# Performance work log

Measured on AMD Instinct MI355X. Metric: run time of the kernel, lower is better.

The kernel has to match this reference:

```python
import jax, jax.numpy as jnp
import numpy as np

B, T, N, F, O = 4, 8192, 64, 16, 32  # batch, timesteps, vertices, in_feat, out_feat


def setup_inputs() -> dict:
    key = jax.random.key(0)
    ks = jax.random.split(key, 8)
    return {
        "x": jax.random.normal(ks[0], (B, T, N * F), dtype=jnp.float32),
        "adj": jax.random.uniform(ks[1], (N, N), dtype=jnp.float32),
        "W1": jax.random.normal(ks[2], (T,), dtype=jnp.float32) / np.sqrt(T).astype(np.float32),
        "W2": jax.random.normal(ks[3], (F, T), dtype=jnp.float32) / np.sqrt(F).astype(np.float32),
        "W3": jax.random.normal(ks[4], (F,), dtype=jnp.float32) / np.sqrt(F).astype(np.float32),
        "bs": jax.random.normal(ks[5], (1, N, N), dtype=jnp.float32) * 0.02,
        "Vs": jax.random.normal(ks[6], (N, N), dtype=jnp.float32) * 0.02,
        "conv_w": jax.random.normal(ks[7], (O, N * F, 3), dtype=jnp.float32) * 0.02,
    }


def reference(x, adj, W1, W2, W3, bs, Vs, conv_w):
    bz, t, _ = x.shape
    x4 = x.reshape(bz, t, N, F)
    xp = jnp.transpose(x4, (0, 2, 3, 1))  # (B, N, F, T)

    # Spatial attention: S in (B, N, N)
    lhs = jnp.einsum('bnft,t->bnf', xp, W1) @ W2          # (B, N, T)
    rhs = jnp.einsum('f,bnft->bnt', W3, xp)               # (B, N, T)
    product = jnp.einsum('bnt,bmt->bnm', lhs, rhs)        # (B, N, N)
    S = jnp.einsum('nm,bmk->bnk', Vs, jax.nn.sigmoid(product + bs))
    S = jax.nn.softmax(S, axis=1)

    # Apply attention over the vertex dim
    xr = jnp.transpose(x4, (0, 1, 3, 2)).reshape(bz, t * F, N)  # (B, T*F, N)
    xm = jnp.einsum('bpn,bnm->bpm', xr, S)                      # (B, T*F, N)
    xf = jnp.transpose(xm.reshape(bz, t, F, N), (0, 2, 1, 3))   # (B, F, T, N)

    # einsum 'bftn,nn->bftn' == scale by diagonal of adj
    xf = xf * jnp.diagonal(adj)                                 # broadcast over N

    xo = jnp.transpose(xf, (0, 2, 3, 1)).reshape(bz, t, N * F)  # (B, T, N*F)

    # Conv1d(kernel=3, padding=1, no bias), channels-last
    out = jax.lax.conv_general_dilated(
        xo, conv_w,
        window_strides=(1,), padding=((1, 1),),
        dimension_numbers=('NWC', 'OIW', 'NWC'))
    return out  # (B, T, O)
```

## Files before the change

kernel.cpp:

```cpp
#include <hip/hip_runtime.h>
#include <hip/hip_bf16.h>

#define B_ 4
#define T_ 8192
#define N_ 64
#define F_ 16
#define O_ 32

typedef _Float16 half8_t __attribute__((ext_vector_type(8)));
typedef _Float16 half4_t __attribute__((ext_vector_type(4)));
typedef float float4_t __attribute__((ext_vector_type(4)));

#define WS_A1G  0
#define WS_SSC  32768
#define WS_WFT  98304
#define WS_P    884736
#define WS_XH   18874368

#define TB_ 32

__global__ __launch_bounds__(256) void kA2(const float* __restrict__ x,
                                           const float* __restrict__ W1,
                                           const float* __restrict__ W2,
                                           const float* __restrict__ W3,
                                           float* __restrict__ P,
                                           _Float16* __restrict__ xh) {
    __shared__ float w2s[16][TB_ + 1];
    __shared__ float w1s[TB_];
    const int b    = blockIdx.x >> 8;
    const int tile = blockIdx.x & 255;
    const int t0   = tile * TB_;
    const int tid  = threadIdx.x;
    const int fq   = tid & 3;

    for (int i = tid; i < 16 * TB_; i += 256) {
        const int f = i >> 5, r = i & 31;
        w2s[f][r] = W2[f * T_ + t0 + r];
    }
    if (tid < TB_) w1s[tid] = W1[t0 + tid];
    __syncthreads();

    float w3v[4];
#pragma unroll
    for (int j = 0; j < 4; ++j) w3v[j] = W3[fq * 4 + j];

    const float* xbase = x + ((size_t)b * T_ + t0) * 1024 + tid * 4;
    _Float16* xhb = xh + ((size_t)b * (T_ + 2) + t0 + 1) * 1024 + tid * 4;
    float4_t accA = {0.f, 0.f, 0.f, 0.f};
    float4_t accG = {0.f, 0.f, 0.f, 0.f};

#pragma unroll
    for (int rb = 0; rb < TB_; rb += 8) {
        float4_t xv[8];
#pragma unroll
        for (int i = 0; i < 8; ++i)
            xv[i] = *(const float4_t*)(xbase + (size_t)(rb + i) * 1024);

        float v[8];
#pragma unroll
        for (int i = 0; i < 8; ++i)
            v[i] = xv[i][0] * w3v[0] + xv[i][1] * w3v[1]
                 + xv[i][2] * w3v[2] + xv[i][3] * w3v[3];
#pragma unroll
        for (int i = 0; i < 8; ++i) v[i] += __shfl_xor(v[i], 1);
#pragma unroll
        for (int i = 0; i < 8; ++i) v[i] += __shfl_xor(v[i], 2);
#pragma unroll
        for (int i = 0; i < 8; ++i) {
            const float w1r = w1s[rb + i];
#pragma unroll
            for (int j = 0; j < 4; ++j) {
                accA[j] += w1r * xv[i][j];
                accG[j] += w2s[fq * 4 + j][rb + i] * v[i];
            }
        }

#pragma unroll
        for (int i = 0; i < 8; ++i) {
            half4_t hv;
            hv[0] = (_Float16)xv[i][0]; hv[1] = (_Float16)xv[i][1];
            hv[2] = (_Float16)xv[i][2]; hv[3] = (_Float16)xv[i][3];
            *(half4_t*)(xhb + (size_t)(rb + i) * 1024) = hv;
        }
    }

    {
        half4_t z = {(_Float16)0.f, (_Float16)0.f, (_Float16)0.f, (_Float16)0.f};
        if (tile == 0)
            *(half4_t*)(xh + (size_t)b * (T_ + 2) * 1024 + tid * 4) = z;
        if (tile == 255)
            *(half4_t*)(xh + ((size_t)b * (T_ + 2) + T_ + 1) * 1024 + tid * 4) = z;
    }

    float* pb = P + (size_t)blockIdx.x * 2048 + tid * 4;
    *(float4_t*)pb          = accA;
    *(float4_t*)(pb + 1024) = accG;
}

__global__ __launch_bounds__(256) void kR(const float* __restrict__ P,
                                          float* __restrict__ A1G) {
    const int b   = blockIdx.x >> 6;
    const int seg = blockIdx.x & 63;
    const int tid = threadIdx.x;
    const int o4  = tid & 7;
    const int g   = tid >> 3;

    const float* base = P + (size_t)b * 256 * 2048 + seg * 32 + o4 * 4;
    float4_t s = {0.f, 0.f, 0.f, 0.f};
#pragma unroll
    for (int tt = 0; tt < 8; ++tt) {
        float4_t v = *(const float4_t*)(base + (size_t)(g * 8 + tt) * 2048);
        s += v;
    }

    __shared__ float4_t red[32][8];
    red[g][o4] = s;
    __syncthreads();
    if (tid < 8) {
        float4_t t = {0.f, 0.f, 0.f, 0.f};
#pragma unroll
        for (int gg = 0; gg < 32; ++gg) t += red[gg][tid];
        *(float4_t*)(A1G + (size_t)b * 2048 + seg * 32 + tid * 4) = t;
    }
}

__global__ __launch_bounds__(256) void kC(const float* __restrict__ A1G,
                                          const float* __restrict__ bs,
                                          const float* __restrict__ Vs,
                                          const float* __restrict__ adj,
                                          float* __restrict__ Ssc) {
    const int b = blockIdx.x;
    __shared__ float a1[64][17], g[64][17];
    __shared__ float sig[64][64];
    __shared__ float vs[64][64];
    __shared__ float redmx[4][64];
    __shared__ float redsm[4][64];
    const int tid = threadIdx.x;

    for (int i = tid; i < 1024; i += 256) {
        a1[i >> 4][i & 15] = A1G[b * 2048 + i];
        g [i >> 4][i & 15] = A1G[b * 2048 + 1024 + i];
    }
    for (int i = tid; i < 4096; i += 256) vs[i >> 6][i & 63] = Vs[i];
    __syncthreads();

#pragma unroll
    for (int i = 0; i < 16; ++i) {
        const int e = tid + 256 * i, r = e >> 6, c = e & 63;
        float p = 0.f;
#pragma unroll
        for (int f = 0; f < 16; ++f) p += a1[r][f] * g[c][f];
        p += bs[e];
        sig[r][c] = 1.f / (1.f + __expf(-p));
    }
    __syncthreads();

    const int gw = tid >> 6;
    const int c  = tid & 63;
    const int r0 = gw * 16;

    float sc_[64];
#pragma unroll
    for (int m = 0; m < 64; ++m) sc_[m] = sig[m][c];

    float acc[16];
#pragma unroll
    for (int rl = 0; rl < 16; ++rl) {
        const float4_t* vr = (const float4_t*)&vs[r0 + rl][0];
        float sA = 0.f, sB = 0.f, sC = 0.f, sD = 0.f;
#pragma unroll
        for (int m4 = 0; m4 < 4; ++m4) {
            float4_t v0 = vr[m4];
            float4_t v1 = vr[m4 + 4];
            float4_t v2 = vr[m4 + 8];
            float4_t v3 = vr[m4 + 12];
#pragma unroll
            for (int j = 0; j < 4; ++j) {
                sA += v0[j] * sc_[m4 * 4 + j];
                sB += v1[j] * sc_[16 + m4 * 4 + j];
                sC += v2[j] * sc_[32 + m4 * 4 + j];
                sD += v3[j] * sc_[48 + m4 * 4 + j];
            }
        }
        acc[rl] = (sA + sB) + (sC + sD);
    }

    float pmax = -1e30f;
#pragma unroll
    for (int rl = 0; rl < 16; ++rl) pmax = fmaxf(pmax, acc[rl]);
    redmx[gw][c] = pmax;
    __syncthreads();
    const float mx = fmaxf(fmaxf(redmx[0][c], redmx[1][c]),
                           fmaxf(redmx[2][c], redmx[3][c]));

    float psum = 0.f;
#pragma unroll
    for (int rl = 0; rl < 16; ++rl) {
        acc[rl] = __expf(acc[rl] - mx);
        psum += acc[rl];
    }
    redsm[gw][c] = psum;
    __syncthreads();
    const float sum = (redsm[0][c] + redsm[1][c]) + (redsm[2][c] + redsm[3][c]);
    const float scl = adj[c * 64 + c] / sum;

#pragma unroll
    for (int rl = 0; rl < 16; ++rl)
        Ssc[b * 4096 + (r0 + rl) * 64 + c] = acc[rl] * scl;
}

__global__ __launch_bounds__(256) void kD(const float* __restrict__ Ssc,
                                          const float* __restrict__ conv_w,
                                          _Float16* __restrict__ Wft) {
    const int b = blockIdx.x >> 5, o = blockIdx.x & 31;
    __shared__ float ssc[4096];
    __shared__ float cw[3072];
    const int tid = threadIdx.x;
    for (int i = tid; i < 4096; i += 256) ssc[i] = Ssc[b * 4096 + i];
    for (int i = tid; i < 3072; i += 256) cw[i] = conv_w[o * 3072 + i];
    __syncthreads();

    const size_t obase = (size_t)(b * 2 + (o >> 4)) * 49152 + (size_t)(o & 15) * 8;

#pragma unroll
    for (int i = 0; i < 12; ++i) {
        const int e = tid + 256 * i;
        const int k = e >> 10, rem = e & 1023, m = rem >> 4, f = rem & 15;
        float s = 0.f;
#pragma unroll
        for (int n = 0; n < 64; ++n) s += cw[(n * 16 + f) * 3 + k] * ssc[m * 64 + n];
        const size_t wi = obase + (size_t)(e >> 5) * 512
                        + (size_t)(((e >> 3) & 3) * 16) * 8 + (e & 7);
        Wft[wi] = (_Float16)s;
    }
}

__global__ __launch_bounds__(256) void kE16(const _Float16* __restrict__ xh,
                                            const _Float16* __restrict__ Wft,
                                            float* __restrict__ out) {
    const int b    = blockIdx.x >> 7;
    const int tile = blockIdx.x & 127;
    const int wave = threadIdx.x >> 6;
    const int lane = threadIdx.x & 63;
    const int q = lane >> 4, l = lane & 15;
    const int t0 = tile * 64 + wave * 16;

    const _Float16* wb0 = Wft + (size_t)(b * 2)     * 49152 + lane * 8;
    const _Float16* wb1 = Wft + (size_t)(b * 2 + 1) * 49152 + lane * 8;
    const _Float16* xb = xh + ((size_t)b * (T_ + 2) + (t0 + l)) * 1024 + q * 8;

    float4_t acc0 = {0.f, 0.f, 0.f, 0.f};
    float4_t acc1 = {0.f, 0.f, 0.f, 0.f};

#pragma unroll 2
    for (int c = 0; c < 32; ++c) {
        const int c0 = c * 32;
#pragma unroll
        for (int kc = 0; kc < 3; ++kc) {
            const int kk = kc * 32 + c;

            half8_t af  = *(const half8_t*)(xb + (size_t)kc * 1024 + c0);
            half8_t bf0 = *(const half8_t*)(wb0 + (size_t)kk * 512);
            half8_t bf1 = *(const half8_t*)(wb1 + (size_t)kk * 512);

            acc0 = __builtin_amdgcn_mfma_f32_16x16x32_f16(af, bf0, acc0, 0, 0, 0);
            acc1 = __builtin_amdgcn_mfma_f32_16x16x32_f16(af, bf1, acc1, 0, 0, 0);
        }
    }

#pragma unroll
    for (int rg = 0; rg < 4; ++rg) {
        const int t = t0 + q * 4 + rg;
        float* op = out + ((size_t)b * T_ + t) * 32;
        op[l]      = acc0[rg];
        op[16 + l] = acc1[rg];
    }
}

extern "C" void kernel_launch(void* const* d_in, const int* in_sizes, int n_in,
                              void* d_out, int out_size, void* d_ws, size_t ws_size,
                              hipStream_t stream) {
    const float* x      = (const float*)d_in[0];
    const float* adj    = (const float*)d_in[1];
    const float* W1     = (const float*)d_in[2];
    const float* W2     = (const float*)d_in[3];
    const float* W3     = (const float*)d_in[4];
    const float* bs     = (const float*)d_in[5];
    const float* Vs     = (const float*)d_in[6];
    const float* conv_w = (const float*)d_in[7];
    float* out = (float*)d_out;

    char* ws = (char*)d_ws;
    float*    A1G = (float*)(ws + WS_A1G);
    float*    Ssc = (float*)(ws + WS_SSC);
    _Float16* Wft = (_Float16*)(ws + WS_WFT);
    float*    P   = (float*)(ws + WS_P);
    _Float16* xh  = (_Float16*)(ws + WS_XH);

    kA2 <<<B_ * (T_ / TB_), 256, 0, stream>>>(x, W1, W2, W3, P, xh);
    kR  <<<B_ * 64,         256, 0, stream>>>(P, A1G);
    kC  <<<B_,              256, 0, stream>>>(A1G, bs, Vs, adj, Ssc);
    kD  <<<B_ * O_,         256, 0, stream>>>(Ssc, conv_w, Wft);
    kE16<<<B_ * (T_ / 64),  256, 0, stream>>>(xh, Wft, out);
}
```

Before: 283.4 us.

## Fuse attention and weight-folding kernels; split conv GEMM waves by output half

Merges the softmax-attention kernel into the conv-weight folding kernel, with each block recomputing the per-batch attention in shared memory. This removes a launch and the global round trip of the scaled attention matrix. The final MFMA kernel now gives each wave one 16-output half over 16 timesteps, doubling the grid for more parallelism. The cost is redundant attention compute across 32 blocks per batch and duplicated input fragment loads across waves.

New measurement: 299.6 us. 1.06x slower.

```diff
diff --git a/kernel.cpp b/kernel.cpp
--- a/kernel.cpp
+++ b/kernel.cpp
@@ -12,7 +12,6 @@
 typedef float float4_t __attribute__((ext_vector_type(4)));
 
 #define WS_A1G  0
-#define WS_SSC  32768
 #define WS_WFT  98304
 #define WS_P    884736
 #define WS_XH   18874368
@@ -124,24 +123,27 @@
     }
 }
 
-__global__ __launch_bounds__(256) void kC(const float* __restrict__ A1G,
-                                          const float* __restrict__ bs,
-                                          const float* __restrict__ Vs,
-                                          const float* __restrict__ adj,
-                                          float* __restrict__ Ssc) {
-    const int b = blockIdx.x;
-    __shared__ float a1[64][17], g[64][17];
-    __shared__ float sig[64][64];
-    __shared__ float vs[64][64];
-    __shared__ float redmx[4][64];
-    __shared__ float redsm[4][64];
+__global__ __launch_bounds__(256) void kCD(const float* __restrict__ A1G,
+                                           const float* __restrict__ bs,
+                                           const float* __restrict__ Vs,
+                                           const float* __restrict__ adj,
+                                           const float* __restrict__ conv_w,
+                                           _Float16* __restrict__ Wft) {
+    const int b = blockIdx.x >> 5, o = blockIdx.x & 31;
+    __shared__ float smem[10880];
+    float* a1  = smem;
+    float* g   = smem + 1088;
+    float* vs  = smem + 2176;
+    float* sig = smem + 6272;
+    float* rmx = smem + 10368;
+    float* rsm = smem + 10624;
     const int tid = threadIdx.x;
 
     for (int i = tid; i < 1024; i += 256) {
-        a1[i >> 4][i & 15] = A1G[b * 2048 + i];
-        g [i >> 4][i & 15] = A1G[b * 2048 + 1024 + i];
-    }
-    for (int i = tid; i < 4096; i += 256) vs[i >> 6][i & 63] = Vs[i];
+        a1[(i >> 4) * 17 + (i & 15)] = A1G[b * 2048 + i];
+        g [(i >> 4) * 17 + (i & 15)] = A1G[b * 2048 + 1024 + i];
+    }
+    for (int i = tid; i < 4096; i += 256) vs[i] = Vs[i];
     __syncthreads();
 
 #pragma unroll
@@ -149,9 +151,9 @@
         const int e = tid + 256 * i, r = e >> 6, c = e & 63;
         float p = 0.f;
 #pragma unroll
-        for (int f = 0; f < 16; ++f) p += a1[r][f] * g[c][f];
+        for (int f = 0; f < 16; ++f) p += a1[r * 17 + f] * g[c * 17 + f];
         p += bs[e];
-        sig[r][c] = 1.f / (1.f + __expf(-p));
+        sig[r * 64 + c] = 1.f / (1.f + __expf(-p));
     }
     __syncthreads();
 
@@ -161,12 +163,12 @@
 
     float sc_[64];
 #pragma unroll
-    for (int m = 0; m < 64; ++m) sc_[m] = sig[m][c];
+    for (int m = 0; m < 64; ++m) sc_[m] = sig[m * 64 + c];
 
     float acc[16];
 #pragma unroll
     for (int rl = 0; rl < 16; ++rl) {
-        const float4_t* vr = (const float4_t*)&vs[r0 + rl][0];
+        const float4_t* vr = (const float4_t*)&vs[(r0 + rl) * 64];
         float sA = 0.f, sB = 0.f, sC = 0.f, sD = 0.f;
 #pragma unroll
         for (int m4 = 0; m4 < 4; ++m4) {
@@ -188,10 +190,10 @@
     float pmax = -1e30f;
 #pragma unroll
     for (int rl = 0; rl < 16; ++rl) pmax = fmaxf(pmax, acc[rl]);
-    redmx[gw][c] = pmax;
-    __syncthreads();
-    const float mx = fmaxf(fmaxf(redmx[0][c], redmx[1][c]),
-                           fmaxf(redmx[2][c], redmx[3][c]));
+    rmx[gw * 64 + c] = pmax;
+    __syncthreads();
+    const float mx = fmaxf(fmaxf(rmx[c], rmx[64 + c]),
+                           fmaxf(rmx[128 + c], rmx[192 + c]));
 
     float psum = 0.f;
 #pragma unroll
@@ -199,29 +201,20 @@
         acc[rl] = __expf(acc[rl] - mx);
         psum += acc[rl];
     }
-    redsm[gw][c] = psum;
-    __syncthreads();
-    const float sum = (redsm[0][c] + redsm[1][c]) + (redsm[2][c] + redsm[3][c]);
+    rsm[gw * 64 + c] = psum;
+    __syncthreads();
+    const float sum = (rsm[c] + rsm[64 + c]) + (rsm[128 + c] + rsm[192 + c]);
     const float scl = adj[c * 64 + c] / sum;
 
+    float* ssc = smem;
+    float* cw  = smem + 4096;
 #pragma unroll
     for (int rl = 0; rl < 16; ++rl)
-        Ssc[b * 4096 + (r0 + rl) * 64 + c] = acc[rl] * scl;
-}
-
-__global__ __launch_bounds__(256) void kD(const float* __restrict__ Ssc,
-                                          const float* __restrict__ conv_w,
-                                          _Float16* __restrict__ Wft) {
-    const int b = blockIdx.x >> 5, o = blockIdx.x & 31;
-    __shared__ float ssc[4096];
-    __shared__ float cw[3072];
-    const int tid = threadIdx.x;
-    for (int i = tid; i < 4096; i += 256) ssc[i] = Ssc[b * 4096 + i];
+        ssc[(r0 + rl) * 64 + c] = acc[rl] * scl;
     for (int i = tid; i < 3072; i += 256) cw[i] = conv_w[o * 3072 + i];
     __syncthreads();
 
     const size_t obase = (size_t)(b * 2 + (o >> 4)) * 49152 + (size_t)(o & 15) * 8;
-
 #pragma unroll
     for (int i = 0; i < 12; ++i) {
         const int e = tid + 256 * i;
@@ -238,42 +231,36 @@
 __global__ __launch_bounds__(256) void kE16(const _Float16* __restrict__ xh,
                                             const _Float16* __restrict__ Wft,
                                             float* __restrict__ out) {
-    const int b    = blockIdx.x >> 7;
-    const int tile = blockIdx.x & 127;
+    const int b    = blockIdx.x >> 8;
+    const int tile = blockIdx.x & 255;
     const int wave = threadIdx.x >> 6;
     const int lane = threadIdx.x & 63;
     const int q = lane >> 4, l = lane & 15;
-    const int t0 = tile * 64 + wave * 16;
-
-    const _Float16* wb0 = Wft + (size_t)(b * 2)     * 49152 + lane * 8;
-    const _Float16* wb1 = Wft + (size_t)(b * 2 + 1) * 49152 + lane * 8;
+    const int tq = wave >> 1, oh = wave & 1;
+    const int t0 = tile * 32 + tq * 16;
+
+    const _Float16* wb = Wft + (size_t)(b * 2 + oh) * 49152 + lane * 8;
     const _Float16* xb = xh + ((size_t)b * (T_ + 2) + (t0 + l)) * 1024 + q * 8;
 
-    float4_t acc0 = {0.f, 0.f, 0.f, 0.f};
-    float4_t acc1 = {0.f, 0.f, 0.f, 0.f};
-
-#pragma unroll 2
+    float4_t acc = {0.f, 0.f, 0.f, 0.f};
+
+#pragma unroll 4
     for (int c = 0; c < 32; ++c) {
         const int c0 = c * 32;
 #pragma unroll
         for (int kc = 0; kc < 3; ++kc) {
             const int kk = kc * 32 + c;
 
-            half8_t af  = *(const half8_t*)(xb + (size_t)kc * 1024 + c0);
-            half8_t bf0 = *(const half8_t*)(wb0 + (size_t)kk * 512);
-            half8_t bf1 = *(const half8_t*)(wb1 + (size_t)kk * 512);
-
-            acc0 = __builtin_amdgcn_mfma_f32_16x16x32_f16(af, bf0, acc0, 0, 0, 0);
-            acc1 = __builtin_amdgcn_mfma_f32_16x16x32_f16(af, bf1, acc1, 0, 0, 0);
+            half8_t af = *(const half8_t*)(xb + (size_t)kc * 1024 + c0);
+            half8_t bf = *(const half8_t*)(wb + (size_t)kk * 512);
+            acc = __builtin_amdgcn_mfma_f32_16x16x32_f16(af, bf, acc, 0, 0, 0);
         }
     }
 
 #pragma unroll
     for (int rg = 0; rg < 4; ++rg) {
         const int t = t0 + q * 4 + rg;
-        float* op = out + ((size_t)b * T_ + t) * 32;
-        op[l]      = acc0[rg];
-        op[16 + l] = acc1[rg];
+        out[((size_t)b * T_ + t) * 32 + oh * 16 + l] = acc[rg];
     }
 }
 
@@ -292,14 +279,12 @@
 
     char* ws = (char*)d_ws;
     float*    A1G = (float*)(ws + WS_A1G);
-    float*    Ssc = (float*)(ws + WS_SSC);
     _Float16* Wft = (_Float16*)(ws + WS_WFT);
     float*    P   = (float*)(ws + WS_P);
     _Float16* xh  = (_Float16*)(ws + WS_XH);
 
     kA2 <<<B_ * (T_ / TB_), 256, 0, stream>>>(x, W1, W2, W3, P, xh);
     kR  <<<B_ * 64,         256, 0, stream>>>(P, A1G);
-    kC  <<<B_,              256, 0, stream>>>(A1G, bs, Vs, adj, Ssc);
-    kD  <<<B_ * O_,         256, 0, stream>>>(Ssc, conv_w, Wft);
-    kE16<<<B_ * (T_ / 64),  256, 0, stream>>>(xh, Wft, out);
-}
+    kCD <<<B_ * O_,         256, 0, stream>>>(A1G, bs, Vs, adj, conv_w, Wft);
+    kE16<<<B_ * (T_ / 32),  256, 0, stream>>>(xh, Wft, out);
+}
```
